# Kernel tuning notes

Hardware: AMD Instinct MI355X
Metric: run time of the kernel (lower is better)

The kernel has to match this reference:

```python
import jax, jax.numpy as jnp
import numpy as np

B, F, N, P, G = 256, 100, 512, 512, 10  # trials, time bins, units, channels, sessions
SCALE = 1.0


def setup_inputs() -> dict:
    key = jax.random.key(0)
    k = jax.random.split(key, 6)
    x = jax.random.normal(k[0], (B, F, N), dtype=jnp.float32)
    eid = jax.random.randint(k[1], (B,), 0, G, dtype=jnp.int32)
    # Per-session stitcher Linear(N -> 2N) and projector Linear(2N -> P)
    W1 = jax.random.normal(k[2], (G, N, 2 * N), dtype=jnp.float32) / np.sqrt(N)
    b1 = jax.random.normal(k[3], (G, 2 * N), dtype=jnp.float32) * 0.01
    W2 = jax.random.normal(k[4], (G, 2 * N, P), dtype=jnp.float32) / np.sqrt(2 * N)
    b2 = jax.random.normal(k[5], (G, P), dtype=jnp.float32) * 0.01
    return {"x": x, "eid": eid, "W1": W1, "b1": b1, "W2": W2, "b2": b2}


def reference(x, eid, W1, b1, W2, b2):
    # Equivalent to the per-eid gather -> Linear -> Softsign*scale -> Linear -> scatter,
    # expressed as batched GEMMs with per-sample gathered weights (same math, vectorized).
    h = jnp.einsum('bfn,bnm->bfm', x, W1[eid]) + b1[eid][:, None, :]   # [B, F, 2N]
    h = (h / (1.0 + jnp.abs(h))) * SCALE                               # Softsign * scale
    out = jnp.einsum('bfm,bmp->bfp', h, W2[eid]) + b2[eid][:, None, :]  # [B, F, P]
    return out
```

## Files before the change

kernel.cpp:

```cpp
#include <hip/hip_runtime.h>
#include <hip/hip_bf16.h>
#include <cstdint>

typedef __attribute__((ext_vector_type(8))) short short8;
typedef __attribute__((ext_vector_type(8))) unsigned short ushort8;
typedef __attribute__((ext_vector_type(4))) float f32x4;

#define B_TRIALS 256
#define F_BINS   100
#define N_UNITS  512
#define P_CH     512
#define G_SESS   10
#define H_DIM    1024
#define TOT_ROWS (B_TRIALS * F_BINS)
#define NT_PAD   216

#define PREP_CASTX_BLOCKS 2048
#define PREP_W1_BLOCKS    5120
#define PREP_W2_BLOCKS    5120
#define PREP_TOTAL (1 + PREP_CASTX_BLOCKS + PREP_W1_BLOCKS + PREP_W2_BLOCKS)

__device__ __forceinline__ unsigned short f2bf(float f) {
  unsigned int u = __builtin_bit_cast(unsigned int, f);
  u += 0x7fffu + ((u >> 16) & 1u);
  return (unsigned short)(u >> 16);
}

__device__ __forceinline__ void gload16(const void* gsrc, void* ldst) {
  __builtin_amdgcn_global_load_lds(
      (const __attribute__((address_space(1))) unsigned int*)gsrc,
      (__attribute__((address_space(3))) unsigned int*)ldst, 16, 0, 0);
}

__device__ __forceinline__ void transpose_tile(const float* __restrict__ src,
                                               unsigned short* __restrict__ dst,
                                               int K, int N, int g, int n0, int k0,
                                               float (*tile)[33]) {
  const float* s = src + (size_t)g * K * N;
  unsigned short* d = dst + (size_t)g * N * K;
  int t = threadIdx.x;
  int r = t >> 3, c = (t & 7) * 4;
  float4 v = *(const float4*)(s + (size_t)(k0 + r) * N + n0 + c);
  tile[r][c + 0] = v.x; tile[r][c + 1] = v.y;
  tile[r][c + 2] = v.z; tile[r][c + 3] = v.w;
  __syncthreads();
  ushort4 o;
  o.x = f2bf(tile[c + 0][r]);
  o.y = f2bf(tile[c + 1][r]);
  o.z = f2bf(tile[c + 2][r]);
  o.w = f2bf(tile[c + 3][r]);
  *(ushort4*)(d + (size_t)(n0 + r) * K + k0 + c) = o;
}

__global__ void prep(const float* __restrict__ x, const int* __restrict__ eid,
                     const float* __restrict__ W1, const float* __restrict__ W2,
                     unsigned short* __restrict__ xb,
                     unsigned short* __restrict__ W1t,
                     unsigned short* __restrict__ W2t,
                     int* __restrict__ rowmap, int* __restrict__ tile_meta) {
  __shared__ float tile[32][33];
  __shared__ int e[B_TRIALS], cnt[G_SESS], off[G_SESS], groff[G_SESS + 1], perm[B_TRIALS];
  const int bid = blockIdx.x;
  const int t = threadIdx.x;

  if (bid == 0) {
    e[t] = eid[t];
    if (t < G_SESS) cnt[t] = 0;
    __syncthreads();
    atomicAdd(&cnt[e[t]], 1);
    __syncthreads();
    if (t == 0) {
      int s = 0, r = 0;
      for (int g = 0; g < G_SESS; g++) {
        off[g] = s; s += cnt[g];
        groff[g] = r; r += cnt[g] * F_BINS;
      }
      groff[G_SESS] = r;
    }
    __syncthreads();
    int g = e[t], rank = 0;
    for (int j = 0; j < t; j++) rank += (e[j] == g);
    perm[off[g] + rank] = t;
    __syncthreads();
    for (int i = t; i < TOT_ROWS; i += 256) {
      int gg = 0;
      while (gg + 1 < G_SESS && i >= groff[gg + 1]) gg++;
      int loc = i - groff[gg];
      rowmap[i] = perm[off[gg] + loc / F_BINS] * F_BINS + loc % F_BINS;
    }
    if (t == 0) {
      int ti = 0;
      for (int g2 = 0; g2 < G_SESS; g2++) {
        int rows = cnt[g2] * F_BINS;
        int base = groff[g2];
        for (int r0 = 0; r0 < rows; r0 += 128) {
          tile_meta[ti * 3 + 0] = g2;
          tile_meta[ti * 3 + 1] = base + r0;
          tile_meta[ti * 3 + 2] = (rows - r0 < 128) ? (rows - r0) : 128;
          ti++;
        }
      }
      for (; ti < NT_PAD; ti++) {
        tile_meta[ti * 3 + 0] = -1; tile_meta[ti * 3 + 1] = 0; tile_meta[ti * 3 + 2] = 0;
      }
    }
  } else if (bid <= PREP_CASTX_BLOCKS) {
    const int n8 = B_TRIALS * F_BINS * N_UNITS / 8;
    int i = (bid - 1) * 256 + t;
    const int stride = PREP_CASTX_BLOCKS * 256;
    for (; i < n8; i += stride) {
      float4 v0 = ((const float4*)x)[(size_t)i * 2];
      float4 v1 = ((const float4*)x)[(size_t)i * 2 + 1];
      ushort8 w;
      w[0] = f2bf(v0.x); w[1] = f2bf(v0.y); w[2] = f2bf(v0.z); w[3] = f2bf(v0.w);
      w[4] = f2bf(v1.x); w[5] = f2bf(v1.y); w[6] = f2bf(v1.z); w[7] = f2bf(v1.w);
      ((ushort8*)xb)[i] = w;
    }
  } else if (bid <= PREP_CASTX_BLOCKS + PREP_W1_BLOCKS) {
    int tt = bid - 1 - PREP_CASTX_BLOCKS;
    int n0 = (tt & 31) * 32, k0 = ((tt >> 5) & 15) * 32, g = tt >> 9;
    transpose_tile(W1, W1t, N_UNITS, H_DIM, g, n0, k0, tile);
  } else {
    int tt = bid - 1 - PREP_CASTX_BLOCKS - PREP_W1_BLOCKS;
    int n0 = (tt & 15) * 32, k0 = ((tt >> 4) & 31) * 32, g = tt >> 9;
    transpose_tile(W2, W2t, H_DIM, P_CH, g, n0, k0, tile);
  }
}


template<int KTOT, int NOUT, int NC, bool IS2>
__global__ __launch_bounds__(256, 4) void gemm_grouped(
    const unsigned short* __restrict__ Asrc,
    const unsigned short* __restrict__ Wt,
    const float* __restrict__ bias,
    const int* __restrict__ rowmap,
    const int* __restrict__ tile_meta,
    unsigned short* __restrict__ hout,
    float* __restrict__ out) {
  __shared__ __align__(16) unsigned short Ash[128 * 64];
  __shared__ __align__(16) unsigned short Bsh[128 * 64];

  const int wg = blockIdx.x;
  const int xcd = wg & 7, slot = wg >> 3;
  const int mt = xcd * (NT_PAD / 8) + slot / NC;
  const int nc = slot % NC;

  const int g = tile_meta[mt * 3 + 0];
  if (g < 0) return;
  const int row0 = tile_meta[mt * 3 + 1];
  const int valid = tile_meta[mt * 3 + 2];
  const int ncol0 = nc * 128;

  const int tid = threadIdx.x;
  const int lane = tid & 63;
  const int w = tid >> 6;
  const int wm = w >> 1, wn = w & 1;
  const int lr = lane & 15, lq = lane >> 4;

  const unsigned short* Wg = Wt + (size_t)g * NOUT * KTOT + (size_t)ncol0 * KTOT;
  const unsigned short* aptr[4];
  const unsigned short* bptr[4];
  {
    int rbase = tid >> 3, q = tid & 7;
#pragma unroll
    for (int it = 0; it < 4; it++) {
      int row = it * 32 + rbase;
      int ks = (q ^ (row & 7)) * 8;
      int grow = row0 + row; if (grow > TOT_ROWS - 1) grow = TOT_ROWS - 1;
      int sr = IS2 ? grow : rowmap[grow];
      aptr[it] = Asrc + (size_t)sr * KTOT + ks;
      bptr[it] = Wg + (size_t)row * KTOT + ks;
    }
  }

  f32x4 acc[4][4];
#pragma unroll
  for (int m = 0; m < 4; m++)
#pragma unroll
    for (int n = 0; n < 4; n++) acc[m][n] = (f32x4){0.f, 0.f, 0.f, 0.f};

  constexpr int NK = KTOT / 64;

  for (int t = 0; t < NK; ++t) {
    const size_t ko = (size_t)t * 64;
    __syncthreads();
#pragma unroll
    for (int it = 0; it < 4; it++) {
      gload16(aptr[it] + ko, &Ash[(it * 256 + (tid & 192)) * 8]);
      gload16(bptr[it] + ko, &Bsh[(it * 256 + (tid & 192)) * 8]);
    }
    asm volatile("s_waitcnt vmcnt(0) lgkmcnt(0)" ::: "memory");
    __syncthreads();

#pragma unroll
    for (int kk = 0; kk < 2; kk++) {
      int kslot = kk * 4 + lq;
      short8 av[4], bv[4];
#pragma unroll
      for (int m = 0; m < 4; m++) {
        int row = wm * 64 + m * 16 + lr;
        av[m] = *(const short8*)&Ash[row * 64 + ((kslot ^ (row & 7)) * 8)];
      }
#pragma unroll
      for (int n = 0; n < 4; n++) {
        int col = wn * 64 + n * 16 + lr;
        bv[n] = *(const short8*)&Bsh[col * 64 + ((kslot ^ (col & 7)) * 8)];
      }
#pragma unroll
      for (int n = 0; n < 4; n++)
#pragma unroll
        for (int m = 0; m < 4; m++)
          acc[m][n] = __builtin_amdgcn_mfma_f32_16x16x32_bf16(av[m], bv[n], acc[m][n], 0, 0, 0);
    }
  }

  float bv4[4];
#pragma unroll
  for (int n = 0; n < 4; n++)
    bv4[n] = bias[(size_t)g * NOUT + ncol0 + wn * 64 + n * 16 + lr];

  if (!IS2) {
#pragma unroll
    for (int m = 0; m < 4; m++)
#pragma unroll
      for (int r4 = 0; r4 < 4; r4++) {
        int lrow = wm * 64 + m * 16 + lq * 4 + r4;
        if (lrow < valid) {
          size_t base = (size_t)(row0 + lrow) * H_DIM + ncol0 + wn * 64 + lr;
#pragma unroll
          for (int n = 0; n < 4; n++) {
            float v = acc[m][n][r4] + bv4[n];
            v = v / (1.0f + fabsf(v));
            hout[base + n * 16] = f2bf(v);
          }
        }
      }
  } else {
#pragma unroll
    for (int m = 0; m < 4; m++)
#pragma unroll
      for (int r4 = 0; r4 < 4; r4++) {
        int lrow = wm * 64 + m * 16 + lq * 4 + r4;
        if (lrow < valid) {
          int orow = rowmap[row0 + lrow];
          size_t base = (size_t)orow * P_CH + ncol0 + wn * 64 + lr;
#pragma unroll
          for (int n = 0; n < 4; n++)
            out[base + n * 16] = acc[m][n][r4] + bv4[n];
        }
      }
  }
}

extern "C" void kernel_launch(void* const* d_in, const int* in_sizes, int n_in,
                              void* d_out, int out_size, void* d_ws, size_t ws_size,
                              hipStream_t stream) {
  const float* x  = (const float*)d_in[0];
  const int* eid  = (const int*)d_in[1];
  const float* W1 = (const float*)d_in[2];
  const float* b1 = (const float*)d_in[3];
  const float* W2 = (const float*)d_in[4];
  const float* b2 = (const float*)d_in[5];
  float* out = (float*)d_out;

  unsigned short* W1t = (unsigned short*)d_ws;
  unsigned short* W2t = W1t + (size_t)G_SESS * H_DIM * N_UNITS;
  unsigned short* h   = W2t + (size_t)G_SESS * P_CH * H_DIM;
  int* rowmap    = (int*)(h + (size_t)TOT_ROWS * H_DIM);
  int* tile_meta = rowmap + TOT_ROWS;
  unsigned short* xb = (unsigned short*)d_out;

  prep<<<PREP_TOTAL, 256, 0, stream>>>(x, eid, W1, W2, xb, W1t, W2t, rowmap, tile_meta);
  gemm_grouped<N_UNITS, H_DIM, 8, false><<<NT_PAD * 8, 256, 0, stream>>>(
      xb, W1t, b1, rowmap, tile_meta, h, out);
  gemm_grouped<H_DIM, P_CH, 4, true><<<NT_PAD * 4, 256, 0, stream>>>(
      h, W2t, b2, rowmap, tile_meta, h, out);
}
```

Baseline: 116.2 us.

## Widen GEMM N-tile to 256 and fold W2 transpose into first GEMM launch

Each GEMM block now computes a 128x256 output tile instead of 128x128, halving the number of N-column blocks and reusing each A tile across twice as many columns. The W2 cast and transpose moves out of the prep kernel into extra blocks appended to the first GEMM launch, so it can overlap with GEMM1 work. The larger accumulator set (4x8 MFMA tiles) and the bigger shared B buffer raise register and LDS use, and launch bounds drop to 2 waves per SIMD, which lowers occupancy and reduces the number of blocks available to fill the GPU.

```diff
diff --git a/kernel.cpp b/kernel.cpp
--- a/kernel.cpp
+++ b/kernel.cpp
@@ -17,8 +17,8 @@
 
 #define PREP_CASTX_BLOCKS 2048
 #define PREP_W1_BLOCKS    5120
-#define PREP_W2_BLOCKS    5120
-#define PREP_TOTAL (1 + PREP_CASTX_BLOCKS + PREP_W1_BLOCKS + PREP_W2_BLOCKS)
+#define PREP_TOTAL (1 + PREP_CASTX_BLOCKS + PREP_W1_BLOCKS)
+#define W2T_BLOCKS        5120
 
 __device__ __forceinline__ unsigned short f2bf(float f) {
   unsigned int u = __builtin_bit_cast(unsigned int, f);
@@ -53,10 +53,9 @@
 }
 
 __global__ void prep(const float* __restrict__ x, const int* __restrict__ eid,
-                     const float* __restrict__ W1, const float* __restrict__ W2,
+                     const float* __restrict__ W1,
                      unsigned short* __restrict__ xb,
                      unsigned short* __restrict__ W1t,
-                     unsigned short* __restrict__ W2t,
                      int* __restrict__ rowmap, int* __restrict__ tile_meta) {
   __shared__ float tile[32][33];
   __shared__ int e[B_TRIALS], cnt[G_SESS], off[G_SESS], groff[G_SESS + 1], perm[B_TRIALS];
@@ -116,29 +115,35 @@
       w[4] = f2bf(v1.x); w[5] = f2bf(v1.y); w[6] = f2bf(v1.z); w[7] = f2bf(v1.w);
       ((ushort8*)xb)[i] = w;
     }
-  } else if (bid <= PREP_CASTX_BLOCKS + PREP_W1_BLOCKS) {
+  } else {
     int tt = bid - 1 - PREP_CASTX_BLOCKS;
     int n0 = (tt & 31) * 32, k0 = ((tt >> 5) & 15) * 32, g = tt >> 9;
     transpose_tile(W1, W1t, N_UNITS, H_DIM, g, n0, k0, tile);
-  } else {
-    int tt = bid - 1 - PREP_CASTX_BLOCKS - PREP_W1_BLOCKS;
-    int n0 = (tt & 15) * 32, k0 = ((tt >> 4) & 31) * 32, g = tt >> 9;
-    transpose_tile(W2, W2t, H_DIM, P_CH, g, n0, k0, tile);
-  }
-}
-
-
-template<int KTOT, int NOUT, int NC, bool IS2>
-__global__ __launch_bounds__(256, 4) void gemm_grouped(
+  }
+}
+
+
+template<int KTOT, int NOUT, int NC, bool IS2, bool XW2>
+__global__ __launch_bounds__(256, 2) void gemm_grouped(
     const unsigned short* __restrict__ Asrc,
     const unsigned short* __restrict__ Wt,
     const float* __restrict__ bias,
     const int* __restrict__ rowmap,
     const int* __restrict__ tile_meta,
     unsigned short* __restrict__ hout,
-    float* __restrict__ out) {
+    float* __restrict__ out,
+    const float* __restrict__ W2src,
+    unsigned short* __restrict__ W2dst) {
   __shared__ __align__(16) unsigned short Ash[128 * 64];
-  __shared__ __align__(16) unsigned short Bsh[128 * 64];
+  __shared__ __align__(16) unsigned short Bsh[256 * 64];
+
+  constexpr int GEMM_BLOCKS = NT_PAD * NC;
+  if (XW2 && blockIdx.x >= GEMM_BLOCKS) {
+    int tt = blockIdx.x - GEMM_BLOCKS;
+    int n0 = (tt & 15) * 32, k0 = ((tt >> 4) & 31) * 32, g = tt >> 9;
+    transpose_tile(W2src, W2dst, H_DIM, P_CH, g, n0, k0, (float(*)[33])Ash);
+    return;
+  }
 
   const int wg = blockIdx.x;
   const int xcd = wg & 7, slot = wg >> 3;
@@ -149,7 +154,7 @@
   if (g < 0) return;
   const int row0 = tile_meta[mt * 3 + 1];
   const int valid = tile_meta[mt * 3 + 2];
-  const int ncol0 = nc * 128;
+  const int ncol0 = nc * 256;
 
   const int tid = threadIdx.x;
   const int lane = tid & 63;
@@ -159,7 +164,7 @@
 
   const unsigned short* Wg = Wt + (size_t)g * NOUT * KTOT + (size_t)ncol0 * KTOT;
   const unsigned short* aptr[4];
-  const unsigned short* bptr[4];
+  const unsigned short* bptr[8];
   {
     int rbase = tid >> 3, q = tid & 7;
 #pragma unroll
@@ -169,15 +174,20 @@
       int grow = row0 + row; if (grow > TOT_ROWS - 1) grow = TOT_ROWS - 1;
       int sr = IS2 ? grow : rowmap[grow];
       aptr[it] = Asrc + (size_t)sr * KTOT + ks;
-      bptr[it] = Wg + (size_t)row * KTOT + ks;
-    }
-  }
-
-  f32x4 acc[4][4];
+    }
+#pragma unroll
+    for (int it = 0; it < 8; it++) {
+      int col = it * 32 + rbase;
+      int ks = (q ^ (col & 7)) * 8;
+      bptr[it] = Wg + (size_t)col * KTOT + ks;
+    }
+  }
+
+  f32x4 acc[4][8];
 #pragma unroll
   for (int m = 0; m < 4; m++)
 #pragma unroll
-    for (int n = 0; n < 4; n++) acc[m][n] = (f32x4){0.f, 0.f, 0.f, 0.f};
+    for (int n = 0; n < 8; n++) acc[m][n] = (f32x4){0.f, 0.f, 0.f, 0.f};
 
   constexpr int NK = KTOT / 64;
 
@@ -185,39 +195,45 @@
     const size_t ko = (size_t)t * 64;
     __syncthreads();
 #pragma unroll
-    for (int it = 0; it < 4; it++) {
+    for (int it = 0; it < 4; it++)
       gload16(aptr[it] + ko, &Ash[(it * 256 + (tid & 192)) * 8]);
+#pragma unroll
+    for (int it = 0; it < 8; it++)
       gload16(bptr[it] + ko, &Bsh[(it * 256 + (tid & 192)) * 8]);
-    }
     asm volatile("s_waitcnt vmcnt(0) lgkmcnt(0)" ::: "memory");
     __syncthreads();
 
 #pragma unroll
     for (int kk = 0; kk < 2; kk++) {
       int kslot = kk * 4 + lq;
-      short8 av[4], bv[4];
+      short8 av[4];
 #pragma unroll
       for (int m = 0; m < 4; m++) {
         int row = wm * 64 + m * 16 + lr;
         av[m] = *(const short8*)&Ash[row * 64 + ((kslot ^ (row & 7)) * 8)];
       }
 #pragma unroll
-      for (int n = 0; n < 4; n++) {
-        int col = wn * 64 + n * 16 + lr;
-        bv[n] = *(const short8*)&Bsh[col * 64 + ((kslot ^ (col & 7)) * 8)];
-      }
-#pragma unroll
-      for (int n = 0; n < 4; n++)
-#pragma unroll
-        for (int m = 0; m < 4; m++)
-          acc[m][n] = __builtin_amdgcn_mfma_f32_16x16x32_bf16(av[m], bv[n], acc[m][n], 0, 0, 0);
-    }
-  }
-
-  float bv4[4];
-#pragma unroll
-  for (int n = 0; n < 4; n++)
-    bv4[n] = bias[(size_t)g * NOUT + ncol0 + wn * 64 + n * 16 + lr];
+      for (int nh = 0; nh < 2; nh++) {
+        short8 bv[4];
+#pragma unroll
+        for (int n = 0; n < 4; n++) {
+          int col = wn * 128 + nh * 64 + n * 16 + lr;
+          bv[n] = *(const short8*)&Bsh[col * 64 + ((kslot ^ (col & 7)) * 8)];
+        }
+#pragma unroll
+        for (int n = 0; n < 4; n++)
+#pragma unroll
+          for (int m = 0; m < 4; m++)
+            acc[m][nh * 4 + n] =
+                __builtin_amdgcn_mfma_f32_16x16x32_bf16(av[m], bv[n], acc[m][nh * 4 + n], 0, 0, 0);
+      }
+    }
+  }
+
+  float bv8[8];
+#pragma unroll
+  for (int j = 0; j < 8; j++)
+    bv8[j] = bias[(size_t)g * NOUT + ncol0 + wn * 128 + (j >> 2) * 64 + (j & 3) * 16 + lr];
 
   if (!IS2) {
 #pragma unroll
@@ -226,12 +242,12 @@
       for (int r4 = 0; r4 < 4; r4++) {
         int lrow = wm * 64 + m * 16 + lq * 4 + r4;
         if (lrow < valid) {
-          size_t base = (size_t)(row0 + lrow) * H_DIM + ncol0 + wn * 64 + lr;
-#pragma unroll
-          for (int n = 0; n < 4; n++) {
-            float v = acc[m][n][r4] + bv4[n];
+          size_t base = (size_t)(row0 + lrow) * H_DIM + ncol0 + wn * 128 + lr;
+#pragma unroll
+          for (int j = 0; j < 8; j++) {
+            float v = acc[m][j][r4] + bv8[j];
             v = v / (1.0f + fabsf(v));
-            hout[base + n * 16] = f2bf(v);
+            hout[base + (j >> 2) * 64 + (j & 3) * 16] = f2bf(v);
           }
         }
       }
@@ -243,10 +259,10 @@
         int lrow = wm * 64 + m * 16 + lq * 4 + r4;
         if (lrow < valid) {
           int orow = rowmap[row0 + lrow];
-          size_t base = (size_t)orow * P_CH + ncol0 + wn * 64 + lr;
-#pragma unroll
-          for (int n = 0; n < 4; n++)
-            out[base + n * 16] = acc[m][n][r4] + bv4[n];
+          size_t base = (size_t)orow * P_CH + ncol0 + wn * 128 + lr;
+#pragma unroll
+          for (int j = 0; j < 8; j++)
+            out[base + (j >> 2) * 64 + (j & 3) * 16] = acc[m][j][r4] + bv8[j];
         }
       }
   }
@@ -270,9 +286,9 @@
   int* tile_meta = rowmap + TOT_ROWS;
   unsigned short* xb = (unsigned short*)d_out;
 
-  prep<<<PREP_TOTAL, 256, 0, stream>>>(x, eid, W1, W2, xb, W1t, W2t, rowmap, tile_meta);
-  gemm_grouped<N_UNITS, H_DIM, 8, false><<<NT_PAD * 8, 256, 0, stream>>>(
-      xb, W1t, b1, rowmap, tile_meta, h, out);
-  gemm_grouped<H_DIM, P_CH, 4, true><<<NT_PAD * 4, 256, 0, stream>>>(
-      h, W2t, b2, rowmap, tile_meta, h, out);
-}
+  prep<<<PREP_TOTAL, 256, 0, stream>>>(x, eid, W1, xb, W1t, rowmap, tile_meta);
+  gemm_grouped<N_UNITS, H_DIM, 4, false, true><<<NT_PAD * 4 + W2T_BLOCKS, 256, 0, stream>>>(
+      xb, W1t, b1, rowmap, tile_meta, h, out, W2, W2t);
+  gemm_grouped<H_DIM, P_CH, 2, true, false><<<NT_PAD * 2, 256, 0, stream>>>(
+      h, W2t, b2, rowmap, tile_meta, h, out, nullptr, nullptr);
+}
```

Result: no change. 117.2 us (+0.8%).
